# Kernel optimization log

Measured on AMD Instinct MI355X. Metric: run time of the kernel, lower is better.

Reference implementation:

```python
import jax, jax.numpy as jnp
import numpy as np

B, T, D = 8, 2048, 1024

def _xavier(key, shape):
    fan_in, fan_out = shape[1], shape[0]
    limit = float(np.sqrt(6.0 / (fan_in + fan_out)))
    return jax.random.uniform(key, shape, jnp.float32, -limit, limit)

def setup_inputs() -> dict:
    key = jax.random.key(0)
    ks = jax.random.split(key, 6)
    x = jax.random.normal(ks[0], (B, T, D), jnp.float32)
    return {
        "x": x,
        "h0": jnp.zeros((B, D), jnp.float32),
        "W_in": _xavier(ks[1], (D, D)),      # in_proj.weight [d_inner, dim]
        "W_alpha": _xavier(ks[2], (D, D)),
        "d_alpha": jnp.full((D,), 0.1, jnp.float32),
        "b_alpha": jnp.full((D,), 2.0, jnp.float32),
        "W_x": _xavier(ks[3], (D, D)),
        "b_v": jnp.zeros((D,), jnp.float32),
        "W_out": _xavier(ks[4], (D, D)),     # out_proj.weight [dim, d_inner]
    }

def _silu(u):
    return u * jax.nn.sigmoid(u)

def reference(x, h0, W_in, W_alpha, d_alpha, b_alpha, W_x, b_v, W_out):
    # in_proj + SiLU: [B,T,D]
    x_proj = _silu(jnp.einsum('btd,ed->bte', x, W_in))
    # to [T,B,D] for the scan
    x_rnn = jnp.transpose(x_proj, (1, 0, 2))
    # precompute per-step gate/value GEMM contributions (as in torch ref)
    alpha_x = jnp.einsum('tbd,ed->tbe', x_rnn, W_alpha)          # [T,B,D]
    v_all = jnp.tanh(jnp.einsum('tbd,ed->tbe', x_rnn, W_x) + b_v)  # [T,B,D]

    def step(h_prev, inputs):
        ax_t, v_t = inputs
        alpha = jax.nn.sigmoid(ax_t + d_alpha * h_prev + b_alpha)
        h_new = alpha * h_prev + (1.0 - alpha) * v_t
        out_t = h_new * _silu(h_new)
        return h_new, out_t

    h_final, cell_out = jax.lax.scan(step, h0, (alpha_x, v_all))  # cell_out: [T,B,D]
    cell_out = jnp.transpose(cell_out, (1, 0, 2))                 # [B,T,D]
    output = jnp.einsum('btd,ed->bte', cell_out, W_out)
    return output, h_final
```

## Files before the change

kernel.cpp:

```cpp
#include <hip/hip_runtime.h>
#include <hip/hip_bf16.h>

typedef __attribute__((ext_vector_type(8))) short short8;
typedef __attribute__((ext_vector_type(4))) short short4v;
typedef __attribute__((ext_vector_type(4))) float f32x4;

#define Dk 1024
#define TT 2048
#define BB 8
#define MROWS (BB * TT)
#define LOG2E 1.44269504088896f

#if defined(__has_builtin)
#if __has_builtin(__builtin_amdgcn_rcpf)
#define FAST_RCP(x) __builtin_amdgcn_rcpf(x)
#endif
#if __has_builtin(__builtin_amdgcn_exp2f)
#define FAST_EXP2(x) __builtin_amdgcn_exp2f(x)
#endif
#endif
#ifndef FAST_RCP
#define FAST_RCP(x) (1.f / (x))
#endif
#ifndef FAST_EXP2
#define FAST_EXP2(x) exp2f(x)
#endif

__device__ __forceinline__ void gload_lds16(const void* g, void* l) {
    __builtin_amdgcn_global_load_lds(
        (const __attribute__((address_space(1))) void*)g,
        (__attribute__((address_space(3))) void*)l, 16, 0, 0);
}

__device__ __forceinline__ float sigmoidf_fast(float x) {
    return FAST_RCP(1.f + FAST_EXP2(-x * LOG2E));
}

__device__ __forceinline__ unsigned short bf16_bits(float x) {
    union { __hip_bfloat16 h; unsigned short u; } c;
    c.h = __float2bfloat16(x);
    return c.u;
}

__global__ __launch_bounds__(256)
void cvt_all(const float* __restrict__ x,
             const float* __restrict__ w0, const float* __restrict__ w1,
             const float* __restrict__ w2, const float* __restrict__ w3,
             __hip_bfloat16* __restrict__ xo,
             __hip_bfloat16* __restrict__ o0, __hip_bfloat16* __restrict__ o1,
             __hip_bfloat16* __restrict__ o2, __hip_bfloat16* __restrict__ o3)
{
    const int bid = blockIdx.x;
    const float* in;
    __hip_bfloat16* out;
    int base;
    if (bid < 16384) {
        in = x; out = xo; base = bid * 1024;
    } else {
        const int wbid  = bid - 16384;
        const int which = wbid >> 10;
        in  = which == 0 ? w0 : which == 1 ? w1 : which == 2 ? w2 : w3;
        out = which == 0 ? o0 : which == 1 ? o1 : which == 2 ? o2 : o3;
        base = (wbid & 1023) * 1024;
    }
    const int i = base + threadIdx.x * 4;
    const float4 v = *(const float4*)(in + i);
    __hip_bfloat16 tmp[4];
    tmp[0] = __float2bfloat16(v.x);
    tmp[1] = __float2bfloat16(v.y);
    tmp[2] = __float2bfloat16(v.z);
    tmp[3] = __float2bfloat16(v.w);
    *(short4v*)(out + i) = *(const short4v*)tmp;
}

template<int EPI>
__global__ __launch_bounds__(512)
void gemm256(const __hip_bfloat16* __restrict__ A,
             const __hip_bfloat16* __restrict__ Bw,
             const float* __restrict__ bias,
             const float* __restrict__ dal,
             void* __restrict__ CoutV)
{
    __shared__ __align__(16) char lds[3 * 32768];

    const int tid  = threadIdx.x;
    const int bid  = blockIdx.x;
    const int nbid = (bid & 7) * 32 + (bid >> 3);
    const int tn   = nbid & 3;
    const int tm   = nbid >> 2;
    const int lane = tid & 63;
    const int w    = tid >> 6;
    const int wm   = w >> 2;
    const int wn   = w & 3;
    const int l15  = lane & 15;
    const int lq   = lane >> 4;

    const size_t baseA = (size_t)(tm * 256) * Dk;
    const __hip_bfloat16* Bp = Bw + (size_t)(tn * 256) * Dk;

    int offA[8], offB[4];
#pragma unroll
    for (int m = 0; m < 8; ++m) {
        const int row = wm * 128 + m * 16 + l15;
        offA[m] = (row * 4 + (lq ^ (row & 3))) * 16;
    }
#pragma unroll
    for (int n = 0; n < 4; ++n) {
        const int row = wn * 64 + n * 16 + l15;
        offB[n] = 16384 + (row * 4 + (lq ^ (row & 3))) * 16;
    }

    auto stageTile = [&](int kt, char* dst) {
#pragma unroll
        for (int j = 0; j < 4; ++j) {
            const int slot = j * 512 + tid;
            const int s    = slot & 1023;
            const int row  = s >> 2;
            const int cb   = (s & 3) ^ (row & 3);
            const __hip_bfloat16* src =
                ((slot >> 10) ? Bp : A + baseA)
                + (size_t)row * Dk + kt * 32 + cb * 8;
            gload_lds16(src, dst + slot * 16);
        }
    };

    f32x4 acc[8][4];
#pragma unroll
    for (int m = 0; m < 8; ++m)
#pragma unroll
        for (int n = 0; n < 4; ++n)
            acc[m][n] = (f32x4){0.f, 0.f, 0.f, 0.f};

    char* cbuf = lds;
    char* nbuf = lds + 32768;
    char* sbuf = lds + 65536;

    stageTile(0, cbuf);
    stageTile(1, nbuf);
    asm volatile("s_waitcnt vmcnt(4)" ::: "memory");
    __builtin_amdgcn_s_barrier();

    for (int t = 0; t < 32; ++t) {
        if (t < 30) stageTile(t + 2, sbuf);

        short8 af[8], bfr[4];
#pragma unroll
        for (int n = 0; n < 4; ++n)
            bfr[n] = *(const short8*)(cbuf + offB[n]);
#pragma unroll
        for (int m = 0; m < 8; ++m)
            af[m] = *(const short8*)(cbuf + offA[m]);

        __builtin_amdgcn_s_setprio(1);
#pragma unroll
        for (int m = 0; m < 8; ++m)
#pragma unroll
            for (int n = 0; n < 4; ++n)
                acc[m][n] = __builtin_amdgcn_mfma_f32_16x16x32_bf16(
                    af[m], bfr[n], acc[m][n], 0, 0, 0);
        __builtin_amdgcn_s_setprio(0);

        if (t < 30) {
            asm volatile("s_waitcnt vmcnt(4)" ::: "memory");
        } else if (t == 30) {
            asm volatile("s_waitcnt vmcnt(0)" ::: "memory");
        }
        if (t < 31) __builtin_amdgcn_s_barrier();

        char* tmp = cbuf; cbuf = nbuf; nbuf = sbuf; sbuf = tmp;
    }

#pragma unroll
    for (int m = 0; m < 8; ++m) {
#pragma unroll
        for (int n = 0; n < 4; ++n) {
            const int col = tn * 256 + wn * 64 + n * 16 + l15;
            float bv_ = 0.f;
            if (EPI == 6 || EPI == 7) bv_ = bias[col];
#pragma unroll
            for (int j = 0; j < 4; ++j) {
                const int rowg = tm * 256 + wm * 128 + m * 16 + lq * 4 + j;
                const size_t idx = (size_t)rowg * Dk + col;
                const float xv = acc[m][n][j];
                if constexpr (EPI == 0) {
                    ((__hip_bfloat16*)CoutV)[idx] =
                        __float2bfloat16(xv * sigmoidf_fast(xv));
                } else if constexpr (EPI == 1) {
                    ((float*)CoutV)[idx] = xv;
                } else if constexpr (EPI == 6) {
                    const float e = FAST_EXP2(-(xv + bv_) * LOG2E);
                    ((unsigned short*)CoutV)[idx * 2] = bf16_bits(e);
                } else {
                    const float y = xv + bv_;
                    const float e = FAST_EXP2(fabsf(y) * (2.f * LOG2E));
                    float tv = 1.f - 2.f * FAST_RCP(e + 1.f);
                    tv = copysignf(tv, y);
                    float nl2 = -dal[col] * LOG2E;
                    if (fabsf(nl2) < 1e-18f) nl2 = -1e-18f;
                    ((unsigned short*)CoutV)[idx * 2 + 1] = bf16_bits(tv * nl2);
                }
            }
        }
    }
}

__global__ __launch_bounds__(192)
void scan_kernel(const unsigned int* __restrict__ EV,
                 const float* __restrict__ h0,
                 const float* __restrict__ dal,
                 __hip_bfloat16* __restrict__ cell, float* __restrict__ hfin)
{
    constexpr int CH  = 64;
    constexpr int NCH = TT / CH;
    __shared__ __align__(16) unsigned int lEV[2][CH * 64];
    __shared__ __align__(16) float        lH [2][CH * 64];

    const int tid  = threadIdx.x;
    const int wave = tid >> 6;
    const int lane = tid & 63;
    const int bx   = blockIdx.x;
    const int b    = bx >> 4;
    const int d0   = (bx & 15) * 64;
    const int d    = d0 + lane;
    const int g    = b * Dk + d;

    float nl2 = -dal[d] * LOG2E;
    if (fabsf(nl2) < 1e-18f) nl2 = -1e-18f;
    const float inv_nl2 = 1.f / nl2;

    const size_t sbase = (size_t)b * TT * Dk + d0;

    if (wave == 0) {
        float ht = h0[g] * nl2;

        const int sl = lane >> 4;
        const int co = (lane & 15) * 4;
        auto issue = [&](int ck, int buf) {
#pragma unroll
            for (int grp = 0; grp < 16; ++grp) {
                const size_t off = sbase + (size_t)(ck * CH + grp * 4 + sl) * Dk + co;
                gload_lds16(EV + off, (void*)&lEV[buf][grp * 256]);
            }
        };

        issue(0, 0);
        for (int k = 0; k < NCH; ++k) {
            const int buf = k & 1;
            asm volatile("s_waitcnt vmcnt(0)" ::: "memory");
            if (k + 1 < NCH) issue(k + 1, buf ^ 1);
            __builtin_amdgcn_sched_barrier(0);

#pragma unroll
            for (int s = 0; s < CH; ++s) {
                const unsigned int wv = lEV[buf][s * 64 + lane];
                const float E  = __uint_as_float(wv << 16);
                const float Vt = __uint_as_float(wv & 0xffff0000u);
                const float u  = FAST_EXP2(ht);
                const float al = FAST_RCP(fmaf(E, u, 1.f));
                ht = fmaf(al, ht - Vt, Vt);
                lH[buf][s * 64 + lane] = ht;
            }
            asm volatile("s_waitcnt lgkmcnt(0)" ::: "memory");
            __builtin_amdgcn_s_barrier();
        }
        hfin[g] = ht * inv_nl2;
    } else {
        const int s0 = (wave - 1) * 32;
        for (int k = 0; k < NCH; ++k) {
            __builtin_amdgcn_s_barrier();
            const int buf = k & 1;
            const size_t cbase = sbase + (size_t)(k * CH) * Dk + lane;
#pragma unroll
            for (int si = 0; si < 32; ++si) {
                const int s = s0 + si;
                const float ht = lH[buf][s * 64 + lane];
                const float h  = ht * inv_nl2;
                const float sg = FAST_RCP(1.f + FAST_EXP2(-h * LOG2E));
                cell[cbase + (size_t)s * Dk] = __float2bfloat16(h * h * sg);
            }
        }
    }
}

extern "C" void kernel_launch(void* const* d_in, const int* in_sizes, int n_in,
                              void* d_out, int out_size, void* d_ws, size_t ws_size,
                              hipStream_t stream)
{
    const float* x     = (const float*)d_in[0];
    const float* h0    = (const float*)d_in[1];
    const float* W_in  = (const float*)d_in[2];
    const float* W_al  = (const float*)d_in[3];
    const float* d_al  = (const float*)d_in[4];
    const float* b_al  = (const float*)d_in[5];
    const float* W_x   = (const float*)d_in[6];
    const float* b_v   = (const float*)d_in[7];
    const float* W_out = (const float*)d_in[8];

    float* out  = (float*)d_out;
    float* hfin = out + (size_t)MROWS * Dk;

    char* ws = (char*)d_ws;
    const size_t bfBuf = (size_t)MROWS * Dk * sizeof(__hip_bfloat16);
    const size_t wBuf  = (size_t)Dk * Dk * sizeof(__hip_bfloat16);

    __hip_bfloat16* xb    = (__hip_bfloat16*)(ws);
    __hip_bfloat16* Winb  = (__hip_bfloat16*)(ws + bfBuf);
    __hip_bfloat16* Walb  = (__hip_bfloat16*)(ws + bfBuf + wBuf);
    __hip_bfloat16* Wxb   = (__hip_bfloat16*)(ws + bfBuf + 2 * wBuf);
    __hip_bfloat16* Woutb = (__hip_bfloat16*)(ws + bfBuf + 3 * wBuf);
    char* rest = ws + bfBuf + 4 * wBuf;
    __hip_bfloat16* xproj = (__hip_bfloat16*)rest;
    unsigned int*   EVb   = (unsigned int*)(rest + bfBuf);

    __hip_bfloat16* cellb = xproj;

    dim3 blk(256);
    cvt_all<<<dim3(16384 + 4096), blk, 0, stream>>>(
        x, W_in, W_al, W_x, W_out, xb, Winb, Walb, Wxb, Woutb);

    dim3 gblk(512), ggrid(256);
    gemm256<0><<<ggrid, gblk, 0, stream>>>(xb,    Winb,  nullptr, nullptr, xproj);
    gemm256<6><<<ggrid, gblk, 0, stream>>>(xproj, Walb,  b_al,    nullptr, EVb);
    gemm256<7><<<ggrid, gblk, 0, stream>>>(xproj, Wxb,   b_v,     d_al,    EVb);
    scan_kernel<<<dim3(128), dim3(192), 0, stream>>>(EVb, h0, d_al, cellb, hfin);
    gemm256<1><<<ggrid, gblk, 0, stream>>>(cellb, Woutb, nullptr, nullptr, out);
}
```

Baseline: 259.7 us.

## Restructure GEMM main loop into 8-wave ping-pong with BK=64 and split staging

Replaces the triple-buffered BK=32 mainloop with a double-buffered BK=64 loop split into four quadrant phases. Each phase interleaves LDS fragment reads, half-tile global-to-LDS staging and MFMA clusters, separated by barriers and lgkmcnt waits. B tiles are prefetched two steps ahead and A one step ahead, using an 8-column XOR swizzle. The goal is to overlap memory traffic with compute and halve loop iterations, at the cost of 128KB of LDS per block and many more barriers per iteration.

```diff
diff --git a/kernel.cpp b/kernel.cpp
--- a/kernel.cpp
+++ b/kernel.cpp
@@ -25,6 +25,10 @@
 #ifndef FAST_EXP2
 #define FAST_EXP2(x) exp2f(x)
 #endif
+
+#define BAR()   __builtin_amdgcn_s_barrier()
+#define LGKM0() do { asm volatile("s_waitcnt lgkmcnt(0)" ::: "memory"); \
+                     __builtin_amdgcn_sched_barrier(0); } while (0)
 
 __device__ __forceinline__ void gload_lds16(const void* g, void* l) {
     __builtin_amdgcn_global_load_lds(
@@ -81,7 +85,7 @@
              const float* __restrict__ dal,
              void* __restrict__ CoutV)
 {
-    __shared__ __align__(16) char lds[3 * 32768];
+    __shared__ __align__(16) char lds[2 * 65536];
 
     const int tid  = threadIdx.x;
     const int bid  = blockIdx.x;
@@ -95,32 +99,25 @@
     const int l15  = lane & 15;
     const int lq   = lane >> 4;
 
-    const size_t baseA = (size_t)(tm * 256) * Dk;
+    const __hip_bfloat16* Ap = A  + (size_t)(tm * 256) * Dk;
     const __hip_bfloat16* Bp = Bw + (size_t)(tn * 256) * Dk;
 
-    int offA[8], offB[4];
-#pragma unroll
-    for (int m = 0; m < 8; ++m) {
-        const int row = wm * 128 + m * 16 + l15;
-        offA[m] = (row * 4 + (lq ^ (row & 3))) * 16;
-    }
-#pragma unroll
-    for (int n = 0; n < 4; ++n) {
-        const int row = wn * 64 + n * 16 + l15;
-        offB[n] = 16384 + (row * 4 + (lq ^ (row & 3))) * 16;
-    }
-
-    auto stageTile = [&](int kt, char* dst) {
-#pragma unroll
-        for (int j = 0; j < 4; ++j) {
-            const int slot = j * 512 + tid;
-            const int s    = slot & 1023;
-            const int row  = s >> 2;
-            const int cb   = (s & 3) ^ (row & 3);
-            const __hip_bfloat16* src =
-                ((slot >> 10) ? Bp : A + baseA)
-                + (size_t)row * Dk + kt * 32 + cb * 8;
-            gload_lds16(src, dst + slot * 16);
+    const int rA = wm * 16384 + l15 * 128;
+    const int rB = 32768 + wn * 8192 + l15 * 128;
+    int c8k[2];
+    c8k[0] = ((lq    ) ^ (l15 & 7)) * 16;
+    c8k[1] = ((lq + 4) ^ (l15 & 7)) * 16;
+
+    const int srow = tid >> 3;
+    const int scol = ((tid & 7) ^ (srow & 7)) * 8;
+
+    auto stageHalf = [&](const __hip_bfloat16* src0, int reg, int h, int kt, int bb) {
+#pragma unroll
+        for (int j = 0; j < 2; ++j) {
+            const int row  = h * 128 + j * 64 + srow;
+            const int slot = h * 1024 + j * 512 + tid;
+            gload_lds16(src0 + (size_t)row * Dk + kt * 64 + scol,
+                        (char*)lds + bb + reg * 32768 + slot * 16);
         }
     };
 
@@ -131,43 +128,99 @@
         for (int n = 0; n < 4; ++n)
             acc[m][n] = (f32x4){0.f, 0.f, 0.f, 0.f};
 
-    char* cbuf = lds;
-    char* nbuf = lds + 32768;
-    char* sbuf = lds + 65536;
-
-    stageTile(0, cbuf);
-    stageTile(1, nbuf);
+    stageHalf(Ap, 0, 0, 0, 0);      stageHalf(Ap, 0, 1, 0, 0);
+    stageHalf(Bp, 1, 0, 0, 0);      stageHalf(Bp, 1, 1, 0, 0);
+    stageHalf(Bp, 1, 0, 1, 65536);  stageHalf(Bp, 1, 1, 1, 65536);
     asm volatile("s_waitcnt vmcnt(4)" ::: "memory");
-    __builtin_amdgcn_s_barrier();
-
-    for (int t = 0; t < 32; ++t) {
-        if (t < 30) stageTile(t + 2, sbuf);
-
-        short8 af[8], bfr[4];
-#pragma unroll
-        for (int n = 0; n < 4; ++n)
-            bfr[n] = *(const short8*)(cbuf + offB[n]);
-#pragma unroll
-        for (int m = 0; m < 8; ++m)
-            af[m] = *(const short8*)(cbuf + offA[m]);
-
+    BAR();
+
+    short8 a[4][2], bfr[4][2];
+
+    for (int t = 0; t < 16; ++t) {
+        const int bb = (t & 1) * 65536;
+        const int nb = bb ^ 65536;
+        const char* cb = (const char*)lds + bb;
+
+#pragma unroll
+        for (int m = 0; m < 4; ++m)
+#pragma unroll
+            for (int kk = 0; kk < 2; ++kk)
+                a[m][kk] = *(const short8*)(cb + rA + m * 2048 + c8k[kk]);
+#pragma unroll
+        for (int n = 0; n < 2; ++n)
+#pragma unroll
+            for (int kk = 0; kk < 2; ++kk)
+                bfr[n][kk] = *(const short8*)(cb + rB + n * 2048 + c8k[kk]);
+        if (t + 1 < 16) stageHalf(Ap, 0, 0, t + 1, nb);
+        BAR(); LGKM0();
         __builtin_amdgcn_s_setprio(1);
 #pragma unroll
-        for (int m = 0; m < 8; ++m)
-#pragma unroll
-            for (int n = 0; n < 4; ++n)
-                acc[m][n] = __builtin_amdgcn_mfma_f32_16x16x32_bf16(
-                    af[m], bfr[n], acc[m][n], 0, 0, 0);
+        for (int m = 0; m < 4; ++m)
+#pragma unroll
+            for (int n = 0; n < 2; ++n)
+#pragma unroll
+                for (int kk = 0; kk < 2; ++kk)
+                    acc[m][n] = __builtin_amdgcn_mfma_f32_16x16x32_bf16(
+                        a[m][kk], bfr[n][kk], acc[m][n], 0, 0, 0);
         __builtin_amdgcn_s_setprio(0);
-
-        if (t < 30) {
+        BAR();
+
+#pragma unroll
+        for (int n = 2; n < 4; ++n)
+#pragma unroll
+            for (int kk = 0; kk < 2; ++kk)
+                bfr[n][kk] = *(const short8*)(cb + rB + n * 2048 + c8k[kk]);
+        if (t + 1 < 16) stageHalf(Ap, 0, 1, t + 1, nb);
+        BAR(); LGKM0();
+        __builtin_amdgcn_s_setprio(1);
+#pragma unroll
+        for (int m = 0; m < 4; ++m)
+#pragma unroll
+            for (int n = 2; n < 4; ++n)
+#pragma unroll
+                for (int kk = 0; kk < 2; ++kk)
+                    acc[m][n] = __builtin_amdgcn_mfma_f32_16x16x32_bf16(
+                        a[m][kk], bfr[n][kk], acc[m][n], 0, 0, 0);
+        __builtin_amdgcn_s_setprio(0);
+        BAR();
+
+#pragma unroll
+        for (int m = 0; m < 4; ++m)
+#pragma unroll
+            for (int kk = 0; kk < 2; ++kk)
+                a[m][kk] = *(const short8*)(cb + rA + (m + 4) * 2048 + c8k[kk]);
+        if (t + 2 < 16) stageHalf(Bp, 1, 0, t + 2, bb);
+        BAR(); LGKM0();
+        __builtin_amdgcn_s_setprio(1);
+#pragma unroll
+        for (int m = 0; m < 4; ++m)
+#pragma unroll
+            for (int n = 0; n < 2; ++n)
+#pragma unroll
+                for (int kk = 0; kk < 2; ++kk)
+                    acc[m + 4][n] = __builtin_amdgcn_mfma_f32_16x16x32_bf16(
+                        a[m][kk], bfr[n][kk], acc[m + 4][n], 0, 0, 0);
+        __builtin_amdgcn_s_setprio(0);
+        BAR();
+
+        if (t + 2 < 16) stageHalf(Bp, 1, 1, t + 2, bb);
+        BAR();
+        __builtin_amdgcn_s_setprio(1);
+#pragma unroll
+        for (int m = 0; m < 4; ++m)
+#pragma unroll
+            for (int n = 2; n < 4; ++n)
+#pragma unroll
+                for (int kk = 0; kk < 2; ++kk)
+                    acc[m + 4][n] = __builtin_amdgcn_mfma_f32_16x16x32_bf16(
+                        a[m][kk], bfr[n][kk], acc[m + 4][n], 0, 0, 0);
+        __builtin_amdgcn_s_setprio(0);
+        if (t < 14) {
             asm volatile("s_waitcnt vmcnt(4)" ::: "memory");
-        } else if (t == 30) {
+        } else if (t == 14) {
             asm volatile("s_waitcnt vmcnt(0)" ::: "memory");
         }
-        if (t < 31) __builtin_amdgcn_s_barrier();
-
-        char* tmp = cbuf; cbuf = nbuf; nbuf = sbuf; sbuf = tmp;
+        BAR();
     }
 
 #pragma unroll
```

New measurement: 246.1 us. 1.06x faster.
